# Kernel optimization log

Measured on AMD Instinct MI355X. Metric: run time of the kernel, lower is better.

The kernel has to match this reference:

```python
import jax, jax.numpy as jnp
import numpy as np

B, T, H, W, C = 4, 128, 100, 464, 128
VOCAB, EMB, HID = 30000, 300, 600


def lstm(x, Wx, Wh, b):
    # Keras LSTM, gate order i, f, c, o; returns all hidden states [B,T,HID]
    bsz = x.shape[0]
    xg = jnp.einsum('bte,eg->btg', x, Wx) + b  # precompute input contribution

    def step(carry, xg_t):
        h, c = carry
        g = xg_t + h @ Wh
        i, f, cc, o = jnp.split(g, 4, axis=-1)
        c = jax.nn.sigmoid(f) * c + jax.nn.sigmoid(i) * jnp.tanh(cc)
        h = jax.nn.sigmoid(o) * jnp.tanh(c)
        return (h, c), h

    init = (jnp.zeros((bsz, HID), x.dtype), jnp.zeros((bsz, HID), x.dtype))
    _, hs = jax.lax.scan(step, init, jnp.swapaxes(xg, 0, 1))
    return jnp.swapaxes(hs, 0, 1)


def reverse_seq(x, lengths):
    # tf.reverse_sequence: reverse first lengths[b] steps, keep the rest
    t = jnp.arange(x.shape[1])[None, :]
    L = lengths[:, None]
    idx = jnp.where(t < L, L - 1 - t, t)
    return jnp.take_along_axis(x, idx[:, :, None], axis=1)


def conv5(x, w, b):
    y = jax.lax.conv_general_dilated(x, w, (1, 1), 'SAME',
                                     dimension_numbers=('NHWC', 'HWIO', 'NHWC'))
    return jax.nn.relu(y + b)


def deconv5(x, w, b):
    y = jax.lax.conv_transpose(x, w, (1, 1), 'SAME',
                               dimension_numbers=('NHWC', 'HWIO', 'NHWC'))
    return jax.nn.relu(y + b)


def setup_inputs():
    key = jax.random.key(0)
    ks = jax.random.split(key, 30)
    s = 0.05
    p = {}
    p['image_embed'] = jax.random.normal(ks[0], (B, H, W, C), jnp.float32)
    p['instructions'] = jax.random.randint(ks[1], (B, T), 1, VOCAB).astype(jnp.int32)
    p['instruction_lengths'] = jax.random.randint(ks[2], (B,), T // 2, T + 1).astype(jnp.int32)
    p['embed_table'] = jax.random.normal(ks[3], (VOCAB, EMB), jnp.float32) * s
    p['fwd_Wx'] = jax.random.normal(ks[4], (EMB, 4 * HID), jnp.float32) * s
    p['fwd_Wh'] = jax.random.normal(ks[5], (HID, 4 * HID), jnp.float32) * s
    p['fwd_b'] = jnp.zeros((4 * HID,), jnp.float32)
    p['bwd_Wx'] = jax.random.normal(ks[6], (EMB, 4 * HID), jnp.float32) * s
    p['bwd_Wh'] = jax.random.normal(ks[7], (HID, 4 * HID), jnp.float32) * s
    p['bwd_b'] = jnp.zeros((4 * HID,), jnp.float32)
    p['k1_W'] = jax.random.normal(ks[8], (HID, C * C), jnp.float32) * s
    p['k1_b'] = jnp.zeros((C * C,), jnp.float32)
    p['k2_W'] = jax.random.normal(ks[9], (HID, C * C), jnp.float32) * s
    p['k2_b'] = jnp.zeros((C * C,), jnp.float32)
    p['conv1_w'] = jax.random.normal(ks[10], (5, 5, C, C), jnp.float32) * s
    p['conv1_b'] = jnp.zeros((C,), jnp.float32)
    p['conv2_w'] = jax.random.normal(ks[11], (5, 5, C, C), jnp.float32) * s
    p['conv2_b'] = jnp.zeros((C,), jnp.float32)
    p['deconv1_w'] = jax.random.normal(ks[12], (5, 5, 2 * C, C), jnp.float32) * s
    p['deconv1_b'] = jnp.zeros((C,), jnp.float32)
    p['deconv2_w'] = jax.random.normal(ks[13], (5, 5, C, C), jnp.float32) * s
    p['deconv2_b'] = jnp.zeros((C,), jnp.float32)
    p['d1_W'] = jax.random.normal(ks[14], (C, C), jnp.float32) * s
    p['d1_b'] = jnp.zeros((C,), jnp.float32)
    p['d2_W'] = jax.random.normal(ks[15], (C, C), jnp.float32) * s
    p['d2_b'] = jnp.zeros((C,), jnp.float32)
    p['out_W'] = jax.random.normal(ks[16], (C, 1), jnp.float32) * s
    return p


def reference(image_embed, instructions, instruction_lengths, embed_table,
              fwd_Wx, fwd_Wh, fwd_b, bwd_Wx, bwd_Wh, bwd_b,
              k1_W, k1_b, k2_W, k2_b,
              conv1_w, conv1_b, conv2_w, conv2_b,
              deconv1_w, deconv1_b, deconv2_w, deconv2_b,
              d1_W, d1_b, d2_W, d2_b, out_W):
    # --- text encoder ---
    text = embed_table[instructions]  # [B,T,EMB]
    fo = lstm(text, fwd_Wx, fwd_Wh, fwd_b)
    rev = reverse_seq(text, instruction_lengths)
    bo = reverse_seq(lstm(rev, bwd_Wx, bwd_Wh, bwd_b), instruction_lengths)
    outs = jnp.concatenate([fo, bo], axis=-1)  # [B,T,1200]
    mask = (jnp.arange(T)[None, :] < instruction_lengths[:, None]).astype(outs.dtype)
    outs = outs * mask[:, :, None]
    text_embed = jnp.mean(outs, axis=1)  # [B,1200]
    te1, te2 = jnp.split(text_embed, 2, axis=-1)
    # dynamic per-example 1x1 kernels [B,Cin,Cout]
    kern1 = (te1 @ k1_W + k1_b).reshape(B, C, C)
    kern2 = (te2 @ k2_W + k2_b).reshape(B, C, C)
    # --- U-Net ---
    f1 = conv5(image_embed, conv1_w, conv1_b)
    f2 = conv5(f1, conv2_w, conv2_b)
    g1 = jnp.einsum('bhwc,bco->bhwo', f1, kern1)  # parallel 1x1 conv
    g2 = jnp.einsum('bhwc,bco->bhwo', f2, kern2)
    h2 = deconv5(g2, deconv2_w, deconv2_b)
    h1 = deconv5(jnp.concatenate([h2, g1], axis=3), deconv1_w, deconv1_b)
    o1 = jax.nn.relu(h1 @ d1_W + d1_b)
    o2 = jax.nn.relu(o1 @ d2_W + d2_b)
    out = (o2 @ out_W)[..., 0].reshape(B, -1)  # [B, H*W]
    return jax.nn.softmax(out, axis=-1)
```

## Files before the change

### kernel.cpp

```cpp
#include <hip/hip_runtime.h>
#include <cmath>

#define BATCH 4
#define TSEQ  128
#define HH    100
#define WW    464
#define CC    128
#define EMBD  300
#define HIDD  600
#define GATE4 2400
#define NPIX  (HH*WW)
#define IMG   ((size_t)BATCH*NPIX*CC)

#define OFF_A  ((size_t)0)
#define OFF_B  (IMG)
#define OFF_C  (2*IMG)
#define OFF_XG (3*IMG)
#define SZ_XG  ((size_t)2*BATCH*TSEQ*GATE4)
#define OFF_H  (OFF_XG + SZ_XG)
#define SZ_H   ((size_t)2*2*BATCH*HIDD)
#define OFF_CS (OFF_H + SZ_H)
#define SZ_CS  ((size_t)2*BATCH*HIDD)
#define OFF_TS (OFF_CS + SZ_CS)
#define SZ_TS  ((size_t)2*BATCH*HIDD)
#define OFF_K  (OFF_TS + SZ_TS)
#define SZ_K   ((size_t)2*BATCH*CC*CC)
#define OFF_W  (OFF_TS + SZ_TS + SZ_K)
#define WSLOT  (25*CC*CC)
#define WELEMS (5*WSLOT)
#define OFF_WH (OFF_W + WELEMS)

typedef _Float16 f16x8 __attribute__((ext_vector_type(8)));
typedef _Float16 f16x4 __attribute__((ext_vector_type(4)));
typedef float    f32x4 __attribute__((ext_vector_type(4)));

__global__ void zero_f(float* p, int n) {
    int i = blockIdx.x*blockDim.x + threadIdx.x;
    if (i < n) p[i] = 0.f;
}

__device__ __forceinline__ void cvt8(float4 v0, float4 v1, f16x8& h, f16x8& l) {
    _Float16 h0=(_Float16)v0.x, h1=(_Float16)v0.y, h2=(_Float16)v0.z, h3=(_Float16)v0.w;
    _Float16 h4=(_Float16)v1.x, h5=(_Float16)v1.y, h6=(_Float16)v1.z, h7=(_Float16)v1.w;
    h = (f16x8){h0,h1,h2,h3,h4,h5,h6,h7};
    l = (f16x8){(_Float16)(v0.x-(float)h0), (_Float16)(v0.y-(float)h1),
                (_Float16)(v0.z-(float)h2), (_Float16)(v0.w-(float)h3),
                (_Float16)(v1.x-(float)h4), (_Float16)(v1.y-(float)h5),
                (_Float16)(v1.z-(float)h6), (_Float16)(v1.w-(float)h7)};
}

__global__ void wcvt(const float* __restrict__ c1, const float* __restrict__ c2,
                     const float* __restrict__ dc2, const float* __restrict__ dc1,
                     _Float16* __restrict__ whi, _Float16* __restrict__ wlo)
{
    int e0 = blockIdx.x*256 + threadIdx.x;
    int slot = e0 / WSLOT;
    int r = e0 % WSLOT;
    int tap = r >> 14;
    int idx = r & 16383;
    int e    = idx & 7;
    int lane = (idx >> 3) & 63;
    int ni   = (idx >> 9) & 3;
    int kt   = (idx >> 11) & 3;
    int wn   = (idx >> 13) & 1;
    int l15 = lane & 15, kg = lane >> 4;
    int oc = wn*64 + ni*16 + l15;
    int ic = kt*32 + kg*8 + e;
    const float* s; size_t si;
    if      (slot == 0) { s = c1;  si = ((size_t)tap*128 + ic)*128 + oc; }
    else if (slot == 1) { s = c2;  si = ((size_t)tap*128 + ic)*128 + oc; }
    else if (slot == 2) { s = dc2; si = ((size_t)tap*128 + ic)*128 + oc; }
    else if (slot == 3) { s = dc1; si = ((size_t)tap*256 + ic)*128 + oc; }
    else                { s = dc1; si = ((size_t)tap*256 + 128 + ic)*128 + oc; }
    float v = s[si];
    _Float16 h  = (_Float16)v;
    _Float16 lo = (_Float16)(v - (float)h);
    whi[e0] = h; wlo[e0] = lo;
}

__global__ void wcvt_head(const float* __restrict__ d1W, const float* __restrict__ d2W,
                          _Float16* __restrict__ whd)
{
    int e0 = blockIdx.x*256 + threadIdx.x;
    int which = e0 >> 14;
    int idx = e0 & 16383;
    int e    = idx & 7;
    int lane = (idx >> 3) & 63;
    int ni   = (idx >> 9) & 7;
    int kt   = (idx >> 12) & 3;
    int l15 = lane & 15, kg = lane >> 4;
    int oc = ni*16 + l15;
    int k  = kt*32 + kg*8 + e;
    const float* W = which ? d2W : d1W;
    float v = W[(size_t)k*CC + oc];
    _Float16 h  = (_Float16)v;
    _Float16 lo = (_Float16)(v - (float)h);
    whd[(size_t)which*32768 + idx]         = h;
    whd[(size_t)which*32768 + 16384 + idx] = lo;
}

__global__ void wh_t(const float* __restrict__ fWh, const float* __restrict__ bWh,
                     float* __restrict__ whT)
{
    int j = blockIdx.x*256 + threadIdx.x;
    int dir = blockIdx.y;
    if (j >= GATE4) return;
    const float* W = dir ? bWh : fWh;
    float* o = whT + ((size_t)dir*GATE4 + j)*HIDD;
    for (int k = 0; k < HIDD; k += 4) {
        float4 v;
        v.x = W[(size_t)k*GATE4 + j];
        v.y = W[(size_t)(k+1)*GATE4 + j];
        v.z = W[(size_t)(k+2)*GATE4 + j];
        v.w = W[(size_t)(k+3)*GATE4 + j];
        *reinterpret_cast<float4*>(o + k) = v;
    }
}

__global__ void embed_xg(const int* __restrict__ instr, const int* __restrict__ lens,
                         const float* __restrict__ etab,
                         const float* __restrict__ fWx, const float* __restrict__ fb,
                         const float* __restrict__ bWx, const float* __restrict__ bb,
                         float* __restrict__ xg)
{
    int gy  = blockIdx.y;
    int dir = gy >> 5;
    int b   = (gy >> 3) & 3;
    int tt  = gy & 7;
    int t0  = tt*16;
    int j   = blockIdx.x*256 + threadIdx.x;
    __shared__ int tok[16];
    __shared__ __attribute__((aligned(16))) float rows_t[EMBD][16];
    int L = lens[b];
    if (threadIdx.x < 16) {
        int t = t0 + threadIdx.x;
        int tsel = (dir == 1 && t < L) ? (L - 1 - t) : t;
        tok[threadIdx.x] = instr[b*TSEQ + tsel];
    }
    __syncthreads();
    for (int idx = threadIdx.x; idx < 16*EMBD; idx += 256) {
        int k = idx >> 4, r = idx & 15;
        rows_t[k][r] = etab[(size_t)tok[r]*EMBD + k];
    }
    __syncthreads();
    if (j >= GATE4) return;
    const float* Wx   = dir ? bWx : fWx;
    const float* bias = dir ? bb  : fb;
    float bv = bias[j];
    float acc[16];
    #pragma unroll
    for (int r = 0; r < 16; ++r) acc[r] = bv;
    for (int k = 0; k < EMBD; ++k) {
        float w = Wx[(size_t)k*GATE4 + j];
        float4 a0 = *reinterpret_cast<const float4*>(&rows_t[k][0]);
        float4 a1 = *reinterpret_cast<const float4*>(&rows_t[k][4]);
        float4 a2 = *reinterpret_cast<const float4*>(&rows_t[k][8]);
        float4 a3 = *reinterpret_cast<const float4*>(&rows_t[k][12]);
        acc[0]+=a0.x*w;  acc[1]+=a0.y*w;  acc[2]+=a0.z*w;  acc[3]+=a0.w*w;
        acc[4]+=a1.x*w;  acc[5]+=a1.y*w;  acc[6]+=a1.z*w;  acc[7]+=a1.w*w;
        acc[8]+=a2.x*w;  acc[9]+=a2.y*w;  acc[10]+=a2.z*w; acc[11]+=a2.w*w;
        acc[12]+=a3.x*w; acc[13]+=a3.y*w; acc[14]+=a3.z*w; acc[15]+=a3.w*w;
    }
    float* o = xg + ((size_t)(dir*BATCH + b)*TSEQ + t0)*GATE4 + j;
    #pragma unroll
    for (int r = 0; r < 16; ++r) o[(size_t)r*GATE4] = acc[r];
}

__global__ __launch_bounds__(256)
void lstm_step2(const float* __restrict__ xg, const float* __restrict__ whT,
                const int* __restrict__ lens,
                float* __restrict__ hbuf, float* __restrict__ cbuf,
                float* __restrict__ tsum, int t)
{
    int blk = blockIdx.x;
    int dir = blk / 150;
    int u   = (blk % 150)*4 + (threadIdx.x >> 6);
    int lane = threadIdx.x & 63;
    __shared__ float hl[BATCH][HIDD];
    const float* hprev = hbuf + (((size_t)(t&1)*2 + dir)*BATCH)*HIDD;
    for (int i = threadIdx.x; i < BATCH*HIDD; i += 256) hl[i/HIDD][i % HIDD] = hprev[i];
    __syncthreads();
    const float* wr = whT + (size_t)dir*GATE4*HIDD;
    float acc[4][4] = {};
    #pragma unroll
    for (int i = 0; i < 10; ++i) {
        int k = i*64 + lane;
        if (k < HIDD) {
            float h0 = hl[0][k], h1 = hl[1][k], h2 = hl[2][k], h3 = hl[3][k];
            #pragma unroll
            for (int g = 0; g < 4; ++g) {
                float w = wr[(size_t)(g*HIDD + u)*HIDD + k];
                acc[g][0] += w*h0; acc[g][1] += w*h1;
                acc[g][2] += w*h2; acc[g][3] += w*h3;
            }
        }
    }
    #pragma unroll
    for (int off = 32; off; off >>= 1) {
        #pragma unroll
        for (int g = 0; g < 4; ++g) {
            acc[g][0] += __shfl_xor(acc[g][0], off, 64);
            acc[g][1] += __shfl_xor(acc[g][1], off, 64);
            acc[g][2] += __shfl_xor(acc[g][2], off, 64);
            acc[g][3] += __shfl_xor(acc[g][3], off, 64);
        }
    }
    if (lane == 0) {
        #pragma unroll
        for (int b = 0; b < 4; ++b) {
            const float* x = xg + ((size_t)(dir*BATCH + b)*TSEQ + t)*GATE4;
            float ai = x[u]          + acc[0][b];
            float af = x[HIDD + u]   + acc[1][b];
            float ac = x[2*HIDD + u] + acc[2][b];
            float ao = x[3*HIDD + u] + acc[3][b];
            size_t ci = ((size_t)dir*BATCH + b)*HIDD + u;
            float cold = cbuf[ci];
            float si = 1.f/(1.f + expf(-ai));
            float sf = 1.f/(1.f + expf(-af));
            float so = 1.f/(1.f + expf(-ao));
            float cnew = sf*cold + si*tanhf(ac);
            float hnew = so*tanhf(cnew);
            cbuf[ci] = cnew;
            hbuf[(((size_t)((t+1)&1)*2 + dir)*BATCH + b)*HIDD + u] = hnew;
            if (t < lens[b]) tsum[ci] += hnew;
        }
    }
}

__global__ void kern_gemm(const float* __restrict__ tsum,
                          const float* __restrict__ k1W, const float* __restrict__ k1b,
                          const float* __restrict__ k2W, const float* __restrict__ k2b,
                          float* __restrict__ kern)
{
    int which = blockIdx.y;
    int co = blockIdx.x*256 + threadIdx.x;
    __shared__ float te[BATCH][HIDD];
    for (int i = threadIdx.x; i < BATCH*HIDD; i += 256) {
        int b = i / HIDD, k = i % HIDD;
        te[b][k] = tsum[((size_t)which*BATCH + b)*HIDD + k]*(1.f/128.f);
    }
    __syncthreads();
    const float* W    = which ? k2W : k1W;
    const float* bias = which ? k2b : k1b;
    float bv = bias[co];
    float a0=bv, a1=bv, a2=bv, a3=bv;
    for (int k = 0; k < HIDD; ++k) {
        float w = W[(size_t)k*16384 + co];
        a0 += te[0][k]*w; a1 += te[1][k]*w; a2 += te[2][k]*w; a3 += te[3][k]*w;
    }
    kern[((size_t)which*BATCH+0)*16384+co] = a0;
    kern[((size_t)which*BATCH+1)*16384+co] = a1;
    kern[((size_t)which*BATCH+2)*16384+co] = a2;
    kern[((size_t)which*BATCH+3)*16384+co] = a3;
}

template<int MODE>
__global__ __launch_bounds__(256)
void conv5m(const float* __restrict__ src, const _Float16* __restrict__ whi,
            const _Float16* __restrict__ wlo, const float* __restrict__ bias,
            float* __restrict__ dst)
{
    __shared__ _Float16 lds[2*20480];
    const int tid = threadIdx.x;
    const int b  = blockIdx.z;
    const int r0 = blockIdx.y*4, p0 = blockIdx.x*16;
    const size_t rowS = (size_t)WW*CC, imgS = (size_t)HH*rowS;
    const float* sb = src + (size_t)b*imgS;

    for (int it = 0; it < 20; ++it) {
        int idx = it*256 + tid;
        int c4  = idx & 31;
        int px  = (idx >> 5) % 20;
        int row = idx / 640;
        int gr = r0 + row - 2, gp = p0 + px - 2;
        float4 v = make_float4(0.f,0.f,0.f,0.f);
        if ((unsigned)gr < HH && (unsigned)gp < WW)
            v = *reinterpret_cast<const float4*>(sb + (size_t)gr*rowS + (size_t)gp*CC + c4*4);
        int pix = row*20 + px;
        int ph  = (pix*128 + c4*4) ^ ((pix & 7) << 3);
        _Float16 h0=(_Float16)v.x, h1=(_Float16)v.y, h2=(_Float16)v.z, h3=(_Float16)v.w;
        f16x4 hv = {h0, h1, h2, h3};
        f16x4 lv = {(_Float16)(v.x-(float)h0), (_Float16)(v.y-(float)h1),
                    (_Float16)(v.z-(float)h2), (_Float16)(v.w-(float)h3)};
        *reinterpret_cast<f16x4*>(&lds[ph]) = hv;
        *reinterpret_cast<f16x4*>(&lds[20480 + ph]) = lv;
    }
    __syncthreads();

    const int lane = tid & 63, w = tid >> 6;
    const int wm = w & 1, wn = w >> 1;
    const int l15 = lane & 15, kg = lane >> 4;

    f32x4 acc[2][4];
    #pragma unroll
    for (int mi = 0; mi < 2; ++mi)
        #pragma unroll
        for (int ni = 0; ni < 4; ++ni)
            acc[mi][ni] = (f32x4){0.f,0.f,0.f,0.f};

    for (int dy = 0; dy < 5; ++dy) {
        for (int dx = 0; dx < 5; ++dx) {
            const int tap = dy*5 + dx;
            const _Float16* wth = whi + ((size_t)tap << 14) + wn*8192 + lane*8;
            const _Float16* wtl = wlo + ((size_t)tap << 14) + wn*8192 + lane*8;
            int pix0 = (wm*2 + dy)*20 + l15 + dx;
            int a0 = pix0*128 + kg*8;       int sw0 = (pix0 & 7) << 3;
            int pix1 = pix0 + 20;
            int a1 = pix1*128 + kg*8;       int sw1 = (pix1 & 7) << 3;
            for (int kt = 0; kt < 4; ++kt) {
                const _Float16* ph = wth + kt*2048;
                const _Float16* pl = wtl + kt*2048;
                f16x8 bh0 = *(const f16x8*)(ph);
                f16x8 bh1 = *(const f16x8*)(ph + 512);
                f16x8 bh2 = *(const f16x8*)(ph + 1024);
                f16x8 bh3 = *(const f16x8*)(ph + 1536);
                f16x8 bl0 = *(const f16x8*)(pl);
                f16x8 bl1 = *(const f16x8*)(pl + 512);
                f16x8 bl2 = *(const f16x8*)(pl + 1024);
                f16x8 bl3 = *(const f16x8*)(pl + 1536);
                f16x8 ah0 = *(const f16x8*)&lds[(a0 + kt*32) ^ sw0];
                f16x8 al0 = *(const f16x8*)&lds[20480 + ((a0 + kt*32) ^ sw0)];
                f16x8 ah1 = *(const f16x8*)&lds[(a1 + kt*32) ^ sw1];
                f16x8 al1 = *(const f16x8*)&lds[20480 + ((a1 + kt*32) ^ sw1)];
#define SPLIT_MFMA(mi, ni, AH, AL, BH, BL)                                          \
    acc[mi][ni] = __builtin_amdgcn_mfma_f32_16x16x32_f16(AH, BH, acc[mi][ni],0,0,0);\
    acc[mi][ni] = __builtin_amdgcn_mfma_f32_16x16x32_f16(AH, BL, acc[mi][ni],0,0,0);\
    acc[mi][ni] = __builtin_amdgcn_mfma_f32_16x16x32_f16(AL, BH, acc[mi][ni],0,0,0);
                SPLIT_MFMA(0,0, ah0, al0, bh0, bl0)
                SPLIT_MFMA(0,1, ah0, al0, bh1, bl1)
                SPLIT_MFMA(0,2, ah0, al0, bh2, bl2)
                SPLIT_MFMA(0,3, ah0, al0, bh3, bl3)
                SPLIT_MFMA(1,0, ah1, al1, bh0, bl0)
                SPLIT_MFMA(1,1, ah1, al1, bh1, bl1)
                SPLIT_MFMA(1,2, ah1, al1, bh2, bl2)
                SPLIT_MFMA(1,3, ah1, al1, bh3, bl3)
#undef SPLIT_MFMA
            }
        }
    }

    #pragma unroll
    for (int ni = 0; ni < 4; ++ni) {
        int oc = wn*64 + ni*16 + l15;
        float bv = (MODE != 0) ? bias[oc] : 0.f;
        #pragma unroll
        for (int mi = 0; mi < 2; ++mi) {
            float* op = dst + (size_t)b*imgS + (size_t)(r0 + wm*2 + mi)*rowS
                            + (size_t)(p0 + kg*4)*CC + oc;
            f32x4 a = acc[mi][ni];
            #pragma unroll
            for (int q = 0; q < 4; ++q) {
                float v = a[q];
                float* ap = op + (size_t)q*CC;
                if (MODE == 0)      *ap = v;
                else if (MODE == 1) *ap = fmaxf(v + bv, 0.f);
                else                *ap = fmaxf(v + *ap + bv, 0.f);
            }
        }
    }
}

__global__ void chanmul(const float* __restrict__ src, const float* __restrict__ kern,
                        float* __restrict__ dst)
{
    __shared__ float kl[CC*CC];
    int b  = blockIdx.y;
    int p0 = blockIdx.x*32;
    const float* kb = kern + (size_t)b*CC*CC;
    for (int i = threadIdx.x; i < CC*CC/4; i += 256)
        reinterpret_cast<float4*>(kl)[i] = reinterpret_cast<const float4*>(kb)[i];
    __syncthreads();
    int ocg = threadIdx.x & 31, pxg = threadIdx.x >> 5;
    int oc0 = ocg*4;
    const float* xs = src + ((size_t)b*NPIX + p0 + pxg*4)*CC;
    float acc[4][4] = {};
    for (int c = 0; c < CC; ++c) {
        float4 wv = *reinterpret_cast<const float4*>(kl + c*CC + oc0);
        #pragma unroll
        for (int pp = 0; pp < 4; ++pp) {
            float xv = xs[(size_t)pp*CC + c];
            acc[pp][0] += xv*wv.x; acc[pp][1] += xv*wv.y;
            acc[pp][2] += xv*wv.z; acc[pp][3] += xv*wv.w;
        }
    }
    #pragma unroll
    for (int pp = 0; pp < 4; ++pp) {
        float* o = dst + ((size_t)b*NPIX + p0 + pxg*4 + pp)*CC + oc0;
        o[0]=acc[pp][0]; o[1]=acc[pp][1]; o[2]=acc[pp][2]; o[3]=acc[pp][3];
    }
}

__global__ __launch_bounds__(256)
void head_mfma(const float* __restrict__ X, const _Float16* __restrict__ whd,
               const float* __restrict__ d1b, const float* __restrict__ d2b,
               const float* __restrict__ oW, float* __restrict__ out)
{
    __shared__ float o1s[4][4096];
    const int tid = threadIdx.x;
    const int lane = tid & 63, w = tid >> 6;
    const int l15 = lane & 15, kg = lane >> 4;
    const size_t pxbase = (size_t)blockIdx.x*128 + w*32;
    float* o1w = o1s[w];

    const _Float16* w1 = whd;
    const _Float16* w2 = whd + 32768;

    f32x4 acc[2][8];
    #pragma unroll
    for (int ni = 0; ni < 8; ++ni) {
        float bv = d1b[ni*16 + l15];
        acc[0][ni] = (f32x4){bv,bv,bv,bv};
        acc[1][ni] = (f32x4){bv,bv,bv,bv};
    }
    #pragma unroll
    for (int kt = 0; kt < 4; ++kt) {
        f16x8 ah0, al0, ah1, al1;
        {
            const float* xp = X + (pxbase + l15)*CC + kt*32 + kg*8;
            cvt8(*(const float4*)xp, *(const float4*)(xp+4), ah0, al0);
            const float* xq = xp + 16*CC;
            cvt8(*(const float4*)xq, *(const float4*)(xq+4), ah1, al1);
        }
        #pragma unroll
        for (int ni = 0; ni < 8; ++ni) {
            const _Float16* bp = w1 + (((size_t)kt*8 + ni)*64 + lane)*8;
            f16x8 bh = *(const f16x8*)bp;
            f16x8 bl = *(const f16x8*)(bp + 16384);
            acc[0][ni] = __builtin_amdgcn_mfma_f32_16x16x32_f16(ah0, bh, acc[0][ni],0,0,0);
            acc[0][ni] = __builtin_amdgcn_mfma_f32_16x16x32_f16(ah0, bl, acc[0][ni],0,0,0);
            acc[0][ni] = __builtin_amdgcn_mfma_f32_16x16x32_f16(al0, bh, acc[0][ni],0,0,0);
            acc[1][ni] = __builtin_amdgcn_mfma_f32_16x16x32_f16(ah1, bh, acc[1][ni],0,0,0);
            acc[1][ni] = __builtin_amdgcn_mfma_f32_16x16x32_f16(ah1, bl, acc[1][ni],0,0,0);
            acc[1][ni] = __builtin_amdgcn_mfma_f32_16x16x32_f16(al1, bh, acc[1][ni],0,0,0);
        }
    }
    #pragma unroll
    for (int mi = 0; mi < 2; ++mi)
        #pragma unroll
        for (int ni = 0; ni < 8; ++ni) {
            f32x4 a = acc[mi][ni];
            #pragma unroll
            for (int q = 0; q < 4; ++q) {
                int px = mi*16 + kg*4 + q;
                int oc = ni*16 + l15;
                o1w[(px*128 + oc) ^ ((px & 7) << 3)] = fmaxf(a[q], 0.f);
            }
        }

    f32x4 acc2[2][8];
    #pragma unroll
    for (int ni = 0; ni < 8; ++ni) {
        float bv = d2b[ni*16 + l15];
        acc2[0][ni] = (f32x4){bv,bv,bv,bv};
        acc2[1][ni] = (f32x4){bv,bv,bv,bv};
    }
    #pragma unroll
    for (int kt = 0; kt < 4; ++kt) {
        f16x8 ah0, al0, ah1, al1;
        {
            int px0 = l15;
            int i0 = (px0*128 + kt*32 + kg*8) ^ ((px0 & 7) << 3);
            cvt8(*(const float4*)&o1w[i0], *(const float4*)&o1w[i0+4], ah0, al0);
            int px1 = 16 + l15;
            int i1 = (px1*128 + kt*32 + kg*8) ^ ((px1 & 7) << 3);
            cvt8(*(const float4*)&o1w[i1], *(const float4*)&o1w[i1+4], ah1, al1);
        }
        #pragma unroll
        for (int ni = 0; ni < 8; ++ni) {
            const _Float16* bp = w2 + (((size_t)kt*8 + ni)*64 + lane)*8;
            f16x8 bh = *(const f16x8*)bp;
            f16x8 bl = *(const f16x8*)(bp + 16384);
            acc2[0][ni] = __builtin_amdgcn_mfma_f32_16x16x32_f16(ah0, bh, acc2[0][ni],0,0,0);
            acc2[0][ni] = __builtin_amdgcn_mfma_f32_16x16x32_f16(ah0, bl, acc2[0][ni],0,0,0);
            acc2[0][ni] = __builtin_amdgcn_mfma_f32_16x16x32_f16(al0, bh, acc2[0][ni],0,0,0);
            acc2[1][ni] = __builtin_amdgcn_mfma_f32_16x16x32_f16(ah1, bh, acc2[1][ni],0,0,0);
            acc2[1][ni] = __builtin_amdgcn_mfma_f32_16x16x32_f16(ah1, bl, acc2[1][ni],0,0,0);
            acc2[1][ni] = __builtin_amdgcn_mfma_f32_16x16x32_f16(al1, bh, acc2[1][ni],0,0,0);
        }
    }

    #pragma unroll
    for (int mi = 0; mi < 2; ++mi) {
        float p0 = 0.f, p1 = 0.f, p2 = 0.f, p3 = 0.f;
        #pragma unroll
        for (int ni = 0; ni < 8; ++ni) {
            float ow = oW[ni*16 + l15];
            f32x4 a = acc2[mi][ni];
            p0 += fmaxf(a[0], 0.f)*ow;
            p1 += fmaxf(a[1], 0.f)*ow;
            p2 += fmaxf(a[2], 0.f)*ow;
            p3 += fmaxf(a[3], 0.f)*ow;
        }
        #pragma unroll
        for (int off = 1; off < 16; off <<= 1) {
            p0 += __shfl_xor(p0, off, 64);
            p1 += __shfl_xor(p1, off, 64);
            p2 += __shfl_xor(p2, off, 64);
            p3 += __shfl_xor(p3, off, 64);
        }
        if (l15 == 0) {
            float* op = out + pxbase + mi*16 + kg*4;
            op[0] = p0; op[1] = p1; op[2] = p2; op[3] = p3;
        }
    }
}

__global__ void softmax_rows(float* __restrict__ out)
{
    int b = blockIdx.x;
    float* row = out + (size_t)b*NPIX;
    __shared__ float red[16];
    float m = -3.4e38f;
    for (int i = threadIdx.x; i < NPIX; i += 1024) m = fmaxf(m, row[i]);
    for (int o = 32; o; o >>= 1) m = fmaxf(m, __shfl_down(m, o, 64));
    if ((threadIdx.x & 63) == 0) red[threadIdx.x >> 6] = m;
    __syncthreads();
    if (threadIdx.x == 0) {
        float mm = red[0];
        for (int i = 1; i < 16; ++i) mm = fmaxf(mm, red[i]);
        red[0] = mm;
    }
    __syncthreads();
    m = red[0];
    __syncthreads();
    float s = 0.f;
    for (int i = threadIdx.x; i < NPIX; i += 1024) s += expf(row[i] - m);
    for (int o = 32; o; o >>= 1) s += __shfl_down(s, o, 64);
    if ((threadIdx.x & 63) == 0) red[threadIdx.x >> 6] = s;
    __syncthreads();
    if (threadIdx.x == 0) {
        float ss = 0.f;
        for (int i = 0; i < 16; ++i) ss += red[i];
        red[0] = ss;
    }
    __syncthreads();
    float inv = 1.f/red[0];
    for (int i = threadIdx.x; i < NPIX; i += 1024) row[i] = expf(row[i] - m)*inv;
}

extern "C" void kernel_launch(void* const* d_in, const int* in_sizes, int n_in,
                              void* d_out, int out_size, void* d_ws, size_t ws_size,
                              hipStream_t stream) {
    (void)in_sizes; (void)n_in; (void)out_size; (void)ws_size;
    const float* img  = (const float*)d_in[0];
    const int* instr  = (const int*)d_in[1];
    const int* lens   = (const int*)d_in[2];
    const float* etab = (const float*)d_in[3];
    const float* fWx  = (const float*)d_in[4];
    const float* fWh  = (const float*)d_in[5];
    const float* fb   = (const float*)d_in[6];
    const float* bWx  = (const float*)d_in[7];
    const float* bWh  = (const float*)d_in[8];
    const float* bb   = (const float*)d_in[9];
    const float* k1W  = (const float*)d_in[10];
    const float* k1b  = (const float*)d_in[11];
    const float* k2W  = (const float*)d_in[12];
    const float* k2b  = (const float*)d_in[13];
    const float* c1w  = (const float*)d_in[14];
    const float* c1b  = (const float*)d_in[15];
    const float* c2w  = (const float*)d_in[16];
    const float* c2b  = (const float*)d_in[17];
    const float* dc1w = (const float*)d_in[18];
    const float* dc1b = (const float*)d_in[19];
    const float* dc2w = (const float*)d_in[20];
    const float* dc2b = (const float*)d_in[21];
    const float* d1W  = (const float*)d_in[22];
    const float* d1b  = (const float*)d_in[23];
    const float* d2W  = (const float*)d_in[24];
    const float* d2b  = (const float*)d_in[25];
    const float* oW   = (const float*)d_in[26];
    float* out = (float*)d_out;
    float* ws  = (float*)d_ws;

    float* A  = ws + OFF_A;
    float* Bb = ws + OFF_B;
    float* Cb = ws + OFF_C;
    float* xg = ws + OFF_XG;
    float* hb = ws + OFF_H;
    float* cb = ws + OFF_CS;
    float* ts = ws + OFF_TS;
    float* kn = ws + OFF_K;
    _Float16* whi = (_Float16*)(ws + OFF_W);
    _Float16* wlo = whi + WELEMS;
    _Float16* whd = (_Float16*)(ws + OFF_WH);
    float* whT = Cb;

    wcvt<<<WELEMS/256, 256, 0, stream>>>(c1w, c2w, dc2w, dc1w, whi, wlo);
    wcvt_head<<<128, 256, 0, stream>>>(d1W, d2W, whd);
    wh_t<<<dim3(10, 2), 256, 0, stream>>>(fWh, bWh, whT);
    zero_f<<<dim3((int)((SZ_H+SZ_CS+SZ_TS+255)/256)), 256, 0, stream>>>(hb, (int)(SZ_H+SZ_CS+SZ_TS));
    embed_xg<<<dim3(10, 64), 256, 0, stream>>>(instr, lens, etab, fWx, fb, bWx, bb, xg);
    for (int t = 0; t < TSEQ; ++t)
        lstm_step2<<<300, 256, 0, stream>>>(xg, whT, lens, hb, cb, ts, t);
    kern_gemm<<<dim3(64, 2), 256, 0, stream>>>(ts, k1W, k1b, k2W, k2b, kn);
    dim3 cgrid(WW/16, HH/4, BATCH);
    conv5m<1><<<cgrid, 256, 0, stream>>>(img, whi + 0*WSLOT, wlo + 0*WSLOT, c1b, A);
    conv5m<1><<<cgrid, 256, 0, stream>>>(A,   whi + 1*WSLOT, wlo + 1*WSLOT, c2b, Bb);
    chanmul<<<dim3(NPIX/32, BATCH), 256, 0, stream>>>(A,  kn, Cb);
    chanmul<<<dim3(NPIX/32, BATCH), 256, 0, stream>>>(Bb, kn + (size_t)BATCH*CC*CC, A);
    conv5m<1><<<cgrid, 256, 0, stream>>>(A,  whi + 2*WSLOT, wlo + 2*WSLOT, dc2b, Bb);
    conv5m<0><<<cgrid, 256, 0, stream>>>(Bb, whi + 3*WSLOT, wlo + 3*WSLOT, dc1b, A);
    conv5m<2><<<cgrid, 256, 0, stream>>>(Cb, whi + 4*WSLOT, wlo + 4*WSLOT, dc1b, A);
    head_mfma<<<1450, 256, 0, stream>>>(A, whd, d1b, d2b, oW, out);
    softmax_rows<<<dim3(BATCH), 1024, 0, stream>>>(out);
}
```

Before: 4.704 ms.

## Persistent LSTM kernel with grid barrier and MFMA split-fp16 channel mixing

Replaces the 128 per-timestep LSTM launches with one persistent kernel. Each block keeps its recurrent weight rows in LDS and its cell state in registers, and a software grid barrier separates timesteps. Separately, the per-example 1x1 channel mixing moves from scalar FP32 FMA to MFMA using hi/lo fp16 splits, with a new conversion kernel that packs the dynamic kernels. The grid barrier depends on all 300 blocks being co-resident, and the split-fp16 path is a small accuracy trade.

```diff
diff --git a/kernel.cpp b/kernel.cpp
--- a/kernel.cpp
+++ b/kernel.cpp
@@ -29,6 +29,7 @@
 #define WSLOT  (25*CC*CC)
 #define WELEMS (5*WSLOT)
 #define OFF_WH (OFF_W + WELEMS)
+#define OFF_KF (OFF_WH + 32768)
 
 typedef _Float16 f16x8 __attribute__((ext_vector_type(8)));
 typedef _Float16 f16x4 __attribute__((ext_vector_type(4)));
@@ -99,6 +100,21 @@
     whd[(size_t)which*32768 + 16384 + idx] = lo;
 }
 
+__global__ void kcvt(const float* __restrict__ kern, _Float16* __restrict__ kf)
+{
+    int e0 = blockIdx.x*256 + threadIdx.x;
+    int wb  = e0 >> 14;
+    int idx = e0 & 16383;
+    int e = idx & 7, lane = (idx >> 3) & 63, ni = (idx >> 9) & 7, kt = (idx >> 12) & 3;
+    int l15 = lane & 15, kg = lane >> 4;
+    int oc = ni*16 + l15;
+    int k  = kt*32 + kg*8 + e;
+    float v = kern[(size_t)wb*16384 + (size_t)k*CC + oc];
+    _Float16 h = (_Float16)v;
+    kf[(size_t)wb*32768 + idx]         = h;
+    kf[(size_t)wb*32768 + 16384 + idx] = (_Float16)(v - (float)h);
+}
+
 __global__ void wh_t(const float* __restrict__ fWh, const float* __restrict__ bWh,
                      float* __restrict__ whT)
 {
@@ -166,65 +182,98 @@
     for (int r = 0; r < 16; ++r) o[(size_t)r*GATE4] = acc[r];
 }
 
+__device__ __forceinline__ void gridbar(int* bar, int nblk) {
+    __threadfence();
+    __syncthreads();
+    if (threadIdx.x == 0) {
+        int g = __hip_atomic_load(&bar[1], __ATOMIC_RELAXED, __HIP_MEMORY_SCOPE_AGENT);
+        int v = __hip_atomic_fetch_add(&bar[0], 1, __ATOMIC_ACQ_REL, __HIP_MEMORY_SCOPE_AGENT);
+        if (v == nblk - 1) {
+            __hip_atomic_store(&bar[0], 0, __ATOMIC_RELAXED, __HIP_MEMORY_SCOPE_AGENT);
+            __hip_atomic_fetch_add(&bar[1], 1, __ATOMIC_RELEASE, __HIP_MEMORY_SCOPE_AGENT);
+        } else {
+            while (__hip_atomic_load(&bar[1], __ATOMIC_ACQUIRE, __HIP_MEMORY_SCOPE_AGENT) == g)
+                __builtin_amdgcn_s_sleep(8);
+        }
+        __threadfence();
+    }
+    __syncthreads();
+}
+
 __global__ __launch_bounds__(256)
-void lstm_step2(const float* __restrict__ xg, const float* __restrict__ whT,
-                const int* __restrict__ lens,
-                float* __restrict__ hbuf, float* __restrict__ cbuf,
-                float* __restrict__ tsum, int t)
-{
-    int blk = blockIdx.x;
-    int dir = blk / 150;
-    int u   = (blk % 150)*4 + (threadIdx.x >> 6);
-    int lane = threadIdx.x & 63;
+void lstm_all(const float* __restrict__ xg, const float* __restrict__ whT,
+              const int* __restrict__ lens,
+              float* __restrict__ hbuf, float* __restrict__ tsum, int* bar)
+{
+    const int blk = blockIdx.x;
+    const int dir = blk / 150;
+    const int wid = threadIdx.x >> 6;
+    const int u   = (blk % 150)*4 + wid;
+    const int lane = threadIdx.x & 63;
+    __shared__ float wlds[4][4][HIDD];
     __shared__ float hl[BATCH][HIDD];
-    const float* hprev = hbuf + (((size_t)(t&1)*2 + dir)*BATCH)*HIDD;
-    for (int i = threadIdx.x; i < BATCH*HIDD; i += 256) hl[i/HIDD][i % HIDD] = hprev[i];
-    __syncthreads();
     const float* wr = whT + (size_t)dir*GATE4*HIDD;
-    float acc[4][4] = {};
-    #pragma unroll
-    for (int i = 0; i < 10; ++i) {
-        int k = i*64 + lane;
-        if (k < HIDD) {
-            float h0 = hl[0][k], h1 = hl[1][k], h2 = hl[2][k], h3 = hl[3][k];
+    #pragma unroll
+    for (int g = 0; g < 4; ++g)
+        for (int k = lane; k < HIDD; k += 64)
+            wlds[wid][g][k] = wr[(size_t)(g*HIDD + u)*HIDD + k];
+    float creg = 0.f, tsreg = 0.f;
+    int Lb = (lane < 4) ? lens[lane] : 0;
+    __syncthreads();
+
+    for (int t = 0; t < TSEQ; ++t) {
+        float xv0=0.f, xv1=0.f, xv2=0.f, xv3=0.f;
+        if (lane < 4) {
+            const float* x = xg + ((size_t)(dir*BATCH + lane)*TSEQ + t)*GATE4;
+            xv0 = x[u]; xv1 = x[HIDD+u]; xv2 = x[2*HIDD+u]; xv3 = x[3*HIDD+u];
+        }
+        const float* hprev = hbuf + (((size_t)(t&1)*2 + dir)*BATCH)*HIDD;
+        for (int i = threadIdx.x; i < BATCH*HIDD; i += 256)
+            hl[i/HIDD][i % HIDD] = hprev[i];
+        __syncthreads();
+        float acc[4][4] = {};
+        #pragma unroll
+        for (int i = 0; i < 10; ++i) {
+            int k = i*64 + lane;
+            if (k < HIDD) {
+                float h0 = hl[0][k], h1 = hl[1][k], h2 = hl[2][k], h3 = hl[3][k];
+                #pragma unroll
+                for (int g = 0; g < 4; ++g) {
+                    float w = wlds[wid][g][k];
+                    acc[g][0] += w*h0; acc[g][1] += w*h1;
+                    acc[g][2] += w*h2; acc[g][3] += w*h3;
+                }
+            }
+        }
+        #pragma unroll
+        for (int off = 32; off; off >>= 1) {
             #pragma unroll
             for (int g = 0; g < 4; ++g) {
-                float w = wr[(size_t)(g*HIDD + u)*HIDD + k];
-                acc[g][0] += w*h0; acc[g][1] += w*h1;
-                acc[g][2] += w*h2; acc[g][3] += w*h3;
+                acc[g][0] += __shfl_xor(acc[g][0], off, 64);
+                acc[g][1] += __shfl_xor(acc[g][1], off, 64);
+                acc[g][2] += __shfl_xor(acc[g][2], off, 64);
+                acc[g][3] += __shfl_xor(acc[g][3], off, 64);
             }
         }
-    }
-    #pragma unroll
-    for (int off = 32; off; off >>= 1) {
-        #pragma unroll
-        for (int g = 0; g < 4; ++g) {
-            acc[g][0] += __shfl_xor(acc[g][0], off, 64);
-            acc[g][1] += __shfl_xor(acc[g][1], off, 64);
-            acc[g][2] += __shfl_xor(acc[g][2], off, 64);
-            acc[g][3] += __shfl_xor(acc[g][3], off, 64);
-        }
-    }
-    if (lane == 0) {
-        #pragma unroll
-        for (int b = 0; b < 4; ++b) {
-            const float* x = xg + ((size_t)(dir*BATCH + b)*TSEQ + t)*GATE4;
-            float ai = x[u]          + acc[0][b];
-            float af = x[HIDD + u]   + acc[1][b];
-            float ac = x[2*HIDD + u] + acc[2][b];
-            float ao = x[3*HIDD + u] + acc[3][b];
-            size_t ci = ((size_t)dir*BATCH + b)*HIDD + u;
-            float cold = cbuf[ci];
+        if (lane < 4) {
+            float g0 = lane==0?acc[0][0]:lane==1?acc[0][1]:lane==2?acc[0][2]:acc[0][3];
+            float g1 = lane==0?acc[1][0]:lane==1?acc[1][1]:lane==2?acc[1][2]:acc[1][3];
+            float g2 = lane==0?acc[2][0]:lane==1?acc[2][1]:lane==2?acc[2][2]:acc[2][3];
+            float g3 = lane==0?acc[3][0]:lane==1?acc[3][1]:lane==2?acc[3][2]:acc[3][3];
+            float ai = xv0 + g0, af = xv1 + g1, ac = xv2 + g2, ao = xv3 + g3;
             float si = 1.f/(1.f + expf(-ai));
             float sf = 1.f/(1.f + expf(-af));
             float so = 1.f/(1.f + expf(-ao));
-            float cnew = sf*cold + si*tanhf(ac);
+            float cnew = sf*creg + si*tanhf(ac);
             float hnew = so*tanhf(cnew);
-            cbuf[ci] = cnew;
-            hbuf[(((size_t)((t+1)&1)*2 + dir)*BATCH + b)*HIDD + u] = hnew;
-            if (t < lens[b]) tsum[ci] += hnew;
-        }
-    }
+            creg = cnew;
+            hbuf[(((size_t)((t+1)&1)*2 + dir)*BATCH + lane)*HIDD + u] = hnew;
+            if (t < Lb) tsreg += hnew;
+        }
+        gridbar(bar, 300);
+    }
+    if (lane < 4)
+        tsum[((size_t)dir*BATCH + lane)*HIDD + u] = tsreg;
 }
 
 __global__ void kern_gemm(const float* __restrict__ tsum,
@@ -360,34 +409,58 @@
     }
 }
 
-__global__ void chanmul(const float* __restrict__ src, const float* __restrict__ kern,
-                        float* __restrict__ dst)
-{
-    __shared__ float kl[CC*CC];
-    int b  = blockIdx.y;
-    int p0 = blockIdx.x*32;
-    const float* kb = kern + (size_t)b*CC*CC;
-    for (int i = threadIdx.x; i < CC*CC/4; i += 256)
-        reinterpret_cast<float4*>(kl)[i] = reinterpret_cast<const float4*>(kb)[i];
-    __syncthreads();
-    int ocg = threadIdx.x & 31, pxg = threadIdx.x >> 5;
-    int oc0 = ocg*4;
-    const float* xs = src + ((size_t)b*NPIX + p0 + pxg*4)*CC;
-    float acc[4][4] = {};
-    for (int c = 0; c < CC; ++c) {
-        float4 wv = *reinterpret_cast<const float4*>(kl + c*CC + oc0);
-        #pragma unroll
-        for (int pp = 0; pp < 4; ++pp) {
-            float xv = xs[(size_t)pp*CC + c];
-            acc[pp][0] += xv*wv.x; acc[pp][1] += xv*wv.y;
-            acc[pp][2] += xv*wv.z; acc[pp][3] += xv*wv.w;
-        }
-    }
-    #pragma unroll
-    for (int pp = 0; pp < 4; ++pp) {
-        float* o = dst + ((size_t)b*NPIX + p0 + pxg*4 + pp)*CC + oc0;
-        o[0]=acc[pp][0]; o[1]=acc[pp][1]; o[2]=acc[pp][2]; o[3]=acc[pp][3];
-    }
+__global__ __launch_bounds__(256)
+void chanmul_mfma(const float* __restrict__ src, const _Float16* __restrict__ kf,
+                  float* __restrict__ dst)
+{
+    const int tid = threadIdx.x;
+    const int lane = tid & 63, w = tid >> 6;
+    const int l15 = lane & 15, kg = lane >> 4;
+    const int b = blockIdx.y;
+    const size_t pxbase = (size_t)blockIdx.x*128 + w*32;
+    if (pxbase >= NPIX) return;
+    const float* X = src + (size_t)b*NPIX*CC;
+    const _Float16* wb = kf + (size_t)b*32768;
+
+    f32x4 acc[2][8];
+    #pragma unroll
+    for (int ni = 0; ni < 8; ++ni) {
+        acc[0][ni] = (f32x4){0.f,0.f,0.f,0.f};
+        acc[1][ni] = (f32x4){0.f,0.f,0.f,0.f};
+    }
+    #pragma unroll
+    for (int kt = 0; kt < 4; ++kt) {
+        f16x8 ah0, al0, ah1, al1;
+        {
+            const float* xp = X + (pxbase + l15)*CC + kt*32 + kg*8;
+            cvt8(*(const float4*)xp, *(const float4*)(xp+4), ah0, al0);
+            const float* xq = xp + 16*CC;
+            cvt8(*(const float4*)xq, *(const float4*)(xq+4), ah1, al1);
+        }
+        #pragma unroll
+        for (int ni = 0; ni < 8; ++ni) {
+            const _Float16* bp = wb + (((size_t)kt*8 + ni)*64 + lane)*8;
+            f16x8 bh = *(const f16x8*)bp;
+            f16x8 bl = *(const f16x8*)(bp + 16384);
+            acc[0][ni] = __builtin_amdgcn_mfma_f32_16x16x32_f16(ah0, bh, acc[0][ni],0,0,0);
+            acc[0][ni] = __builtin_amdgcn_mfma_f32_16x16x32_f16(ah0, bl, acc[0][ni],0,0,0);
+            acc[0][ni] = __builtin_amdgcn_mfma_f32_16x16x32_f16(al0, bh, acc[0][ni],0,0,0);
+            acc[1][ni] = __builtin_amdgcn_mfma_f32_16x16x32_f16(ah1, bh, acc[1][ni],0,0,0);
+            acc[1][ni] = __builtin_amdgcn_mfma_f32_16x16x32_f16(ah1, bl, acc[1][ni],0,0,0);
+            acc[1][ni] = __builtin_amdgcn_mfma_f32_16x16x32_f16(al1, bh, acc[1][ni],0,0,0);
+        }
+    }
+    #pragma unroll
+    for (int mi = 0; mi < 2; ++mi)
+        #pragma unroll
+        for (int ni = 0; ni < 8; ++ni) {
+            f32x4 a = acc[mi][ni];
+            #pragma unroll
+            for (int q = 0; q < 4; ++q) {
+                size_t px = pxbase + mi*16 + kg*4 + q;
+                dst[((size_t)b*NPIX + px)*CC + ni*16 + l15] = a[q];
+            }
+        }
 }
 
 __global__ __launch_bounds__(256)
@@ -577,27 +650,28 @@
     float* Cb = ws + OFF_C;
     float* xg = ws + OFF_XG;
     float* hb = ws + OFF_H;
-    float* cb = ws + OFF_CS;
+    int*   bar = (int*)(ws + OFF_CS);
     float* ts = ws + OFF_TS;
     float* kn = ws + OFF_K;
     _Float16* whi = (_Float16*)(ws + OFF_W);
     _Float16* wlo = whi + WELEMS;
     _Float16* whd = (_Float16*)(ws + OFF_WH);
+    _Float16* kf  = (_Float16*)(ws + OFF_KF);
     float* whT = Cb;
 
     wcvt<<<WELEMS/256, 256, 0, stream>>>(c1w, c2w, dc2w, dc1w, whi, wlo);
     wcvt_head<<<128, 256, 0, stream>>>(d1W, d2W, whd);
     wh_t<<<dim3(10, 2), 256, 0, stream>>>(fWh, bWh, whT);
-    zero_f<<<dim3((int)((SZ_H+SZ_CS+SZ_TS+255)/256)), 256, 0, stream>>>(hb, (int)(SZ_H+SZ_CS+SZ_TS));
+    zero_f<<<dim3((int)((SZ_H + 8 + 255)/256)), 256, 0, stream>>>(hb, (int)(SZ_H + 8));
     embed_xg<<<dim3(10, 64), 256, 0, stream>>>(instr, lens, etab, fWx, fb, bWx, bb, xg);
-    for (int t = 0; t < TSEQ; ++t)
-        lstm_step2<<<300, 256, 0, stream>>>(xg, whT, lens, hb, cb, ts, t);
+    lstm_all<<<300, 256, 0, stream>>>(xg, whT, lens, hb, ts, bar);
     kern_gemm<<<dim3(64, 2), 256, 0, stream>>>(ts, k1W, k1b, k2W, k2b, kn);
+    kcvt<<<512, 256, 0, stream>>>(kn, kf);
     dim3 cgrid(WW/16, HH/4, BATCH);
     conv5m<1><<<cgrid, 256, 0, stream>>>(img, whi + 0*WSLOT, wlo + 0*WSLOT, c1b, A);
     conv5m<1><<<cgrid, 256, 0, stream>>>(A,   whi + 1*WSLOT, wlo + 1*WSLOT, c2b, Bb);
-    chanmul<<<dim3(NPIX/32, BATCH), 256, 0, stream>>>(A,  kn, Cb);
-    chanmul<<<dim3(NPIX/32, BATCH), 256, 0, stream>>>(Bb, kn + (size_t)BATCH*CC*CC, A);
+    chanmul_mfma<<<dim3(363, BATCH), 256, 0, stream>>>(A,  kf,           Cb);
+    chanmul_mfma<<<dim3(363, BATCH), 256, 0, stream>>>(Bb, kf + 4*32768, A);
     conv5m<1><<<cgrid, 256, 0, stream>>>(A,  whi + 2*WSLOT, wlo + 2*WSLOT, dc2b, Bb);
     conv5m<0><<<cgrid, 256, 0, stream>>>(Bb, whi + 3*WSLOT, wlo + 3*WSLOT, dc1b, A);
     conv5m<2><<<cgrid, 256, 0, stream>>>(Cb, whi + 4*WSLOT, wlo + 4*WSLOT, dc1b, A);
```

Result: slower. 11.18 ms (+137.7%).
